# Optimization experiments

Hardware: AMD Instinct MI355X
Metric: run time of the kernel (lower is better)

The kernel has to match this reference:

```python
import jax, jax.numpy as jnp
import numpy as np

N_VAR = 2048   # number of variable nodes
DEG = 4        # edges per variable node
N_EDGE = N_VAR * DEG  # 8192 expanded/duplicated edge messages
BATCH = 32
DENSITY = 8.0 / N_EDGE  # sparse Tanner-style edge-edge connectivity


def setup_inputs() -> dict:
    key = jax.random.key(0)
    k1, k2, k3 = jax.random.split(key, 3)
    inp = jax.random.normal(k1, (BATCH, N_EDGE), dtype=jnp.float32)
    llr = jax.random.normal(k2, (BATCH, N_VAR), dtype=jnp.float32)
    # binary sparse mask [E_out, E_in]
    mask = (jax.random.uniform(k3, (N_EDGE, N_EDGE)) < DENSITY).astype(jnp.float32)
    # llr_expander: one-hot rows mapping each edge to its variable node [E, N_VAR]
    var_idx = jnp.tile(jnp.arange(N_VAR), DEG)
    llr_expander = jax.nn.one_hot(var_idx, N_VAR, dtype=jnp.float32)
    # learned params, initialized as in the module (ones, pre-masked)
    input_weight = mask * jnp.ones((N_EDGE, N_EDGE), dtype=jnp.float32)
    llr_weight = jnp.ones((1, N_VAR), dtype=jnp.float32)
    return {"input": inp, "input_weight": input_weight, "mask": mask,
            "llr": llr, "llr_weight": llr_weight, "llr_expander": llr_expander}


def reference(input, input_weight, mask, llr, llr_weight, llr_expander):
    # x = 0.5 * ( expand(w_llr * llr) + input @ (mask * W).T )
    weighted_input = input @ (mask * input_weight).T          # [B, E]
    expanded_llr = (llr_weight * llr) @ llr_expander.T        # [B, E]
    return 0.5 * (expanded_llr + weighted_input)
```

## Files before the change

kernel.cpp:

```cpp
#include <hip/hip_runtime.h>


#define N_VAR  2048
#define N_EDGE 8192
#define BATCH  32
#define BLOCK  256
#define CAP    32
#define BB     4

typedef unsigned int u32x4 __attribute__((ext_vector_type(4)));

__global__ __launch_bounds__(BLOCK) void bp_scan(
    const float* __restrict__ mask,
    unsigned*    __restrict__ cnt,
    unsigned*    __restrict__ cols)
{
    const int wave = threadIdx.x >> 6;
    const int lane = threadIdx.x & 63;
    const int row  = blockIdx.x * (BLOCK / 64) + wave;

    const u32x4* __restrict__ mrow = (const u32x4*)(mask + (size_t)row * N_EDGE);
    unsigned* __restrict__ rcols = cols + (size_t)row * CAP;

    const unsigned long long lt_mask = (1ull << lane) - 1ull;
    unsigned total = 0;

    u32x4 buf[2][BB];
    #pragma unroll
    for (int r = 0; r < BB; ++r)
        buf[0][r] = __builtin_nontemporal_load(&mrow[r * 64 + lane]);

    #pragma unroll
    for (int k = 0; k < 8; ++k) {
        const int cur = k & 1;
        if (k < 7) {
            #pragma unroll
            for (int r = 0; r < BB; ++r)
                buf[cur ^ 1][r] = __builtin_nontemporal_load(
                    &mrow[((k + 1) * BB + r) * 64 + lane]);
        }
        #pragma unroll
        for (int r = 0; r < BB; ++r) {
            const u32x4 v = buf[cur][r];
            if (__ballot((v.x | v.y | v.z | v.w) != 0u)) {
                const unsigned c[4] = { v.x, v.y, v.z, v.w };
                const int colbase = ((k * BB + r) * 64 + lane) * 4;
                #pragma unroll
                for (int j = 0; j < 4; ++j) {
                    const bool hit = (c[j] != 0u);
                    const unsigned long long bal = __ballot(hit);
                    if (bal) {
                        if (hit) {
                            const unsigned idx =
                                total + (unsigned)__popcll(bal & lt_mask);
                            if (idx < CAP)
                                rcols[idx] = (unsigned)(colbase + j);
                        }
                        total += (unsigned)__popcll(bal);
                    }
                }
            }
        }
    }

    if (lane == 0) cnt[row] = (total < CAP) ? total : CAP;
}

__global__ __launch_bounds__(BLOCK) void bp_acc(
    const float* __restrict__ input,
    const float* __restrict__ weight,
    const float* __restrict__ llr,
    const float* __restrict__ llr_w,
    const unsigned* __restrict__ cnt,
    const unsigned* __restrict__ cols,
    float* __restrict__ out)
{
    const int wave = threadIdx.x >> 6;
    const int lane = threadIdx.x & 63;
    const int row  = blockIdx.x * (BLOCK / 64) + wave;
    const int b    = lane & (BATCH - 1);

    const int n = (int)cnt[row];
    int   c = 0;
    float w = 0.0f;
    if (lane < n) {
        c = (int)cols[(size_t)row * CAP + lane];
        w = weight[(size_t)row * N_EDGE + c];
    }

    float acc = 0.0f;
    for (int i = 0; i < n; ++i) {
        const float wb = __shfl(w, i);
        const int   cb = __shfl(c, i);
        acc = fmaf(wb, input[(size_t)b * N_EDGE + cb], acc);
    }

    if (lane < BATCH) {
        const int v = row & (N_VAR - 1);
        const float llr_term = llr_w[v] * llr[(size_t)b * N_VAR + v];
        out[(size_t)b * N_EDGE + row] = 0.5f * (acc + llr_term);
    }
}

extern "C" void kernel_launch(void* const* d_in, const int* in_sizes, int n_in,
                              void* d_out, int out_size, void* d_ws, size_t ws_size,
                              hipStream_t stream) {
    const float* input  = (const float*)d_in[0];
    const float* weight = (const float*)d_in[1];
    const float* mask   = (const float*)d_in[2];
    const float* llr    = (const float*)d_in[3];
    const float* llr_w  = (const float*)d_in[4];
    float* out = (float*)d_out;

    unsigned* cnt  = (unsigned*)d_ws;
    unsigned* cols = (unsigned*)((char*)d_ws + N_EDGE * 4);

    const int grid = N_EDGE / (BLOCK / 64);
    bp_scan<<<grid, BLOCK, 0, stream>>>(mask, cnt, cols);
    bp_acc <<<grid, BLOCK, 0, stream>>>(input, weight, llr, llr_w, cnt, cols, out);
}
```

Before: 482.4 us.

## Flatten mask scan across all threads and scatter hits with atomics

The mask scan no longer assigns one wave per row. The whole mask is now streamed as one flat grid-stride array: each thread keeps up to 8 hits in registers and then appends them to per-row column lists with atomicAdd. A small init kernel zeroes the counters, and the accumulate kernel clamps the count to CAP. The aim is fully coalesced streaming with fewer blocks and no per-column ballots. In exchange, column order within a row becomes nondeterministic, which can change float summation order, and any thread hitting more than 8 nonzeros silently drops the extras.

```diff
diff --git a/kernel.cpp b/kernel.cpp
--- a/kernel.cpp
+++ b/kernel.cpp
@@ -4,69 +4,78 @@
 #define N_VAR  2048
 #define N_EDGE 8192
 #define BATCH  32
-#define BLOCK  256
 #define CAP    32
+#define SCAN_BLOCKS 2048
+#define LANES  (SCAN_BLOCKS * 256)
+#define TOTAL_U4 (N_EDGE * (N_EDGE / 4))
+#define ITERS  (TOTAL_U4 / LANES)
 #define BB     4
 
 typedef unsigned int u32x4 __attribute__((ext_vector_type(4)));
 
-__global__ __launch_bounds__(BLOCK) void bp_scan(
+__global__ __launch_bounds__(256) void bp_init(unsigned* __restrict__ cnt) {
+    cnt[blockIdx.x * 256 + threadIdx.x] = 0u;
+}
+
+__global__ __launch_bounds__(256) void bp_scan(
     const float* __restrict__ mask,
     unsigned*    __restrict__ cnt,
     unsigned*    __restrict__ cols)
 {
-    const int wave = threadIdx.x >> 6;
-    const int lane = threadIdx.x & 63;
-    const int row  = blockIdx.x * (BLOCK / 64) + wave;
+    const unsigned gid = blockIdx.x * 256 + threadIdx.x;
+    const u32x4* __restrict__ m4 = (const u32x4*)mask;
 
-    const u32x4* __restrict__ mrow = (const u32x4*)(mask + (size_t)row * N_EDGE);
-    unsigned* __restrict__ rcols = cols + (size_t)row * CAP;
-
-    const unsigned long long lt_mask = (1ull << lane) - 1ull;
-    unsigned total = 0;
+    unsigned nh = 0;
+    unsigned h0=0,h1=0,h2=0,h3=0,h4=0,h5=0,h6=0,h7=0;
 
     u32x4 buf[2][BB];
     #pragma unroll
     for (int r = 0; r < BB; ++r)
-        buf[0][r] = __builtin_nontemporal_load(&mrow[r * 64 + lane]);
+        buf[0][r] = __builtin_nontemporal_load(&m4[(size_t)r * LANES + gid]);
 
     #pragma unroll
-    for (int k = 0; k < 8; ++k) {
+    for (int k = 0; k < ITERS / BB; ++k) {
         const int cur = k & 1;
-        if (k < 7) {
+        if (k < ITERS / BB - 1) {
             #pragma unroll
             for (int r = 0; r < BB; ++r)
                 buf[cur ^ 1][r] = __builtin_nontemporal_load(
-                    &mrow[((k + 1) * BB + r) * 64 + lane]);
+                    &m4[(size_t)((k + 1) * BB + r) * LANES + gid]);
         }
         #pragma unroll
         for (int r = 0; r < BB; ++r) {
             const u32x4 v = buf[cur][r];
-            if (__ballot((v.x | v.y | v.z | v.w) != 0u)) {
+            if (v.x | v.y | v.z | v.w) {
+                const unsigned f0 = ((unsigned)(k * BB + r) * LANES + gid) * 4u;
                 const unsigned c[4] = { v.x, v.y, v.z, v.w };
-                const int colbase = ((k * BB + r) * 64 + lane) * 4;
                 #pragma unroll
                 for (int j = 0; j < 4; ++j) {
-                    const bool hit = (c[j] != 0u);
-                    const unsigned long long bal = __ballot(hit);
-                    if (bal) {
-                        if (hit) {
-                            const unsigned idx =
-                                total + (unsigned)__popcll(bal & lt_mask);
-                            if (idx < CAP)
-                                rcols[idx] = (unsigned)(colbase + j);
-                        }
-                        total += (unsigned)__popcll(bal);
+                    if (c[j] != 0u) {
+                        const unsigned f = f0 + (unsigned)j;
+                        h0 = (nh == 0u) ? f : h0;  h1 = (nh == 1u) ? f : h1;
+                        h2 = (nh == 2u) ? f : h2;  h3 = (nh == 3u) ? f : h3;
+                        h4 = (nh == 4u) ? f : h4;  h5 = (nh == 5u) ? f : h5;
+                        h6 = (nh == 6u) ? f : h6;  h7 = (nh == 7u) ? f : h7;
+                        ++nh;
                     }
                 }
             }
         }
     }
 
-    if (lane == 0) cnt[row] = (total < CAP) ? total : CAP;
+    const unsigned nf = (nh < 8u) ? nh : 8u;
+    for (unsigned i = 0; i < nf; ++i) {
+        const unsigned f = (i == 0u) ? h0 : (i == 1u) ? h1 : (i == 2u) ? h2 :
+                           (i == 3u) ? h3 : (i == 4u) ? h4 : (i == 5u) ? h5 :
+                           (i == 6u) ? h6 : h7;
+        const unsigned row = f >> 13;
+        const unsigned col = f & (N_EDGE - 1u);
+        const unsigned pos = atomicAdd(&cnt[row], 1u);
+        if (pos < CAP) cols[(size_t)row * CAP + pos] = col;
+    }
 }
 
-__global__ __launch_bounds__(BLOCK) void bp_acc(
+__global__ __launch_bounds__(256) void bp_acc(
     const float* __restrict__ input,
     const float* __restrict__ weight,
     const float* __restrict__ llr,
@@ -77,10 +86,10 @@
 {
     const int wave = threadIdx.x >> 6;
     const int lane = threadIdx.x & 63;
-    const int row  = blockIdx.x * (BLOCK / 64) + wave;
+    const int row  = blockIdx.x * 4 + wave;
     const int b    = lane & (BATCH - 1);
 
-    const int n = (int)cnt[row];
+    const int n = min((int)cnt[row], CAP);
     int   c = 0;
     float w = 0.0f;
     if (lane < n) {
@@ -115,7 +124,8 @@
     unsigned* cnt  = (unsigned*)d_ws;
     unsigned* cols = (unsigned*)((char*)d_ws + N_EDGE * 4);
 
-    const int grid = N_EDGE / (BLOCK / 64);
-    bp_scan<<<grid, BLOCK, 0, stream>>>(mask, cnt, cols);
-    bp_acc <<<grid, BLOCK, 0, stream>>>(input, weight, llr, llr_w, cnt, cols, out);
+    bp_init<<<N_EDGE / 256, 256, 0, stream>>>(cnt);
+    bp_scan<<<SCAN_BLOCKS, 256, 0, stream>>>(mask, cnt, cols);
+    bp_acc <<<N_EDGE / 4, 256, 0, stream>>>(input, weight, llr, llr_w,
+                                            cnt, cols, out);
 }
```

Result: slower. 497.3 us (+3.1%).
